# Performance work log

Measured on AMD Instinct MI355X. Metric: run time of the kernel, lower is better.

## Reference

```python
import math
import jax, jax.numpy as jnp
import numpy as np

D_MODEL = 512
NHEAD = 8
D_HEAD = D_MODEL // NHEAD
TEMP = 0.8
B, LQ, LK = 16, 512, 1024
NEG = -1.0e9


def setup_inputs() -> dict:
    key = jax.random.key(0)
    ks = jax.random.split(key, 12)
    s = 1.0 / math.sqrt(D_MODEL)
    return {
        "Q_src": jax.random.normal(ks[0], (B, LQ, D_MODEL), jnp.float32),
        "KV_src": jax.random.normal(ks[1], (B, LK, D_MODEL), jnp.float32),
        "key_gate": jax.random.uniform(ks[2], (B, LK), jnp.float32, 1e-3, 1.0),
        "key_padding_mask": jax.random.randint(ks[3], (B, LK), 0, 2, jnp.int32),
        "Wq": jax.random.normal(ks[4], (D_MODEL, D_MODEL), jnp.float32) * s,
        "bq": jnp.zeros((D_MODEL,), jnp.float32),
        "Wk": jax.random.normal(ks[5], (D_MODEL, D_MODEL), jnp.float32) * s,
        "bk": jnp.zeros((D_MODEL,), jnp.float32),
        "Wv": jax.random.normal(ks[6], (D_MODEL, D_MODEL), jnp.float32) * s,
        "bv": jnp.zeros((D_MODEL,), jnp.float32),
        "Wo": jax.random.normal(ks[7], (D_MODEL, D_MODEL), jnp.float32) * s,
        "bo": jnp.zeros((D_MODEL,), jnp.float32),
    }


def reference(Q_src, KV_src, key_gate, key_padding_mask, Wq, bq, Wk, bk, Wv, bv, Wo, bo):
    b, lq, _ = Q_src.shape
    lk = KV_src.shape[1]
    # projections -> [B, H, L, Dh]
    q = (Q_src @ Wq + bq).reshape(b, lq, NHEAD, D_HEAD).transpose(0, 2, 1, 3)
    k = (KV_src @ Wk + bk).reshape(b, lk, NHEAD, D_HEAD).transpose(0, 2, 1, 3)
    v = (KV_src @ Wv + bv).reshape(b, lk, NHEAD, D_HEAD).transpose(0, 2, 1, 3)
    # scores with log-gate bias [B, H, Lq, Lk]
    logits = jnp.einsum("bhqd,bhkd->bhqk", q, k) / math.sqrt(D_HEAD)
    logits = logits + jnp.log(key_gate)[:, None, None, :]
    pad = (key_padding_mask == 0)[:, None, None, :]
    logits = jnp.where(pad, NEG, logits) / TEMP
    attn = jax.nn.softmax(logits, axis=-1)
    ctx = jnp.einsum("bhqk,bhkd->bhqd", attn, v)
    ctx = ctx.transpose(0, 2, 1, 3).reshape(b, lq, D_MODEL)
    return ctx @ Wo + bo
```

## Files before the change

### kernel.cpp

```cpp
#include <hip/hip_runtime.h>
#include <math.h>

typedef __bf16 bf16;
typedef __bf16 bf16x8 __attribute__((ext_vector_type(8)));
typedef __bf16 bf16x4 __attribute__((ext_vector_type(4)));
typedef __bf16 bf16x2 __attribute__((ext_vector_type(2)));
typedef float  f32x4  __attribute__((ext_vector_type(4)));
typedef unsigned int uint;

#define SCQ2 0.22542110f
#define SMREF 16.0f

#define VMC(n) asm volatile("s_waitcnt vmcnt(" #n ")" ::: "memory")
#define BARR do { __builtin_amdgcn_s_barrier(); __builtin_amdgcn_sched_barrier(0); } while (0)

#if __has_builtin(__builtin_amdgcn_exp2f)
#define EXP2F __builtin_amdgcn_exp2f
#else
#define EXP2F exp2f
#endif

__device__ __forceinline__ void gload16(const void* g, void* l) {
  __builtin_amdgcn_global_load_lds((const __attribute__((address_space(1))) void*)g,
                                   (__attribute__((address_space(3))) void*)l, 16, 0, 0);
}

__device__ __forceinline__ uint pk2(float a, float b) {
  bf16x2 t = {(bf16)a, (bf16)b};
  return __builtin_bit_cast(uint, t);
}

union V8 { bf16x8 v; bf16x4 h[2]; uint u[4]; };

__global__ void prep_k(const float* __restrict__ Wq, const float* __restrict__ Wk,
                       const float* __restrict__ Wv, const float* __restrict__ Wo,
                       bf16* __restrict__ Tq, bf16* __restrict__ Tkv, bf16* __restrict__ To,
                       const float* __restrict__ gate, const int* __restrict__ mask,
                       float* __restrict__ gfac,
                       const float* __restrict__ Qs, const float* __restrict__ KVs,
                       bf16* __restrict__ Qsb, bf16* __restrict__ KVb) {
  const int bid = blockIdx.x, tid = threadIdx.x;
  if (bid < 256) {
    const int w = bid >> 6, t = bid & 63;
    const float* W = (w == 0) ? Wq : (w == 1) ? Wk : (w == 2) ? Wv : Wo;
    bf16* T = (w == 0) ? Tq : (w == 3) ? To : Tkv;
    const int ro = (w == 2) ? 512 : 0;
    const int k0 = (t >> 3) * 64, n0 = (t & 7) * 64;
    __shared__ bf16 tl[64][72];
#pragma unroll
    for (int i = 0; i < 16; i++) {
      int s = i * 256 + tid;
      int r = s >> 6, c = s & 63;
      tl[r][c] = (bf16)W[(size_t)(k0 + r) * 512 + n0 + c];
    }
    __syncthreads();
#pragma unroll
    for (int i = 0; i < 16; i++) {
      int s = i * 256 + tid;
      int r = s >> 6, c = s & 63;
      T[(size_t)(ro + n0 + r) * 512 + k0 + c] = tl[c][r];
    }
  } else if (bid < 320) {
    int i = (bid - 256) * 256 + tid;
    gfac[i] = mask[i] ? __expf(1.25f * __logf(gate[i])) : 0.0f;
  } else {
    const float* s;
    bf16* d;
    size_t i;
    if (bid < 2368) { s = Qs; d = Qsb; i = ((size_t)(bid - 320) * 256 + tid) * 8; }
    else            { s = KVs; d = KVb; i = ((size_t)(bid - 2368) * 256 + tid) * 8; }
    f32x4 a = *(const f32x4*)(s + i);
    f32x4 b = *(const f32x4*)(s + i + 4);
    bf16x8 o = {(bf16)a[0], (bf16)a[1], (bf16)a[2], (bf16)a[3],
                (bf16)b[0], (bf16)b[1], (bf16)b[2], (bf16)b[3]};
    *(bf16x8*)(d + i) = o;
  }
}

__global__ __launch_bounds__(512, 2) void gemm_kv8(
    const bf16* __restrict__ A, const bf16* __restrict__ Bt,
    const float* __restrict__ kb, const float* __restrict__ vb,
    const float* __restrict__ gfac, bf16* __restrict__ K_out, bf16* __restrict__ V_out) {
  const int tid = threadIdx.x, w = tid >> 6, l = tid & 63;
  const int lg = l >> 4, lr = l & 15;
  const int bid = (int)(blockIdx.x & 7) * 32 + (int)(blockIdx.x >> 3);
  const int bm = (bid >> 2) * 256;
  const int bn = (bid & 3) * 256;
  const int wm = w >> 2, wn = w & 3;

  __shared__ __align__(16) bf16 AB[2][16384];

  const int lrow = l >> 2;
  const int cs = (l & 3) ^ ((l >> 3) & 3);

  f32x4 acc[8][4];
#pragma unroll
  for (int i = 0; i < 8; i++)
#pragma unroll
    for (int j = 0; j < 4; j++) acc[i][j] = (f32x4){0.f, 0.f, 0.f, 0.f};

  auto stA = [&](int p, int u, int kt) {
    const int rb = (w >> 2) * 128 + u * 64 + (w & 3) * 16;
    gload16(A + (size_t)(bm + rb + lrow) * 512 + kt * 32 + cs * 8, &AB[p][rb * 32]);
  };
  auto stB = [&](int p, int u, int kt) {
    const int rb = (w >> 1) * 64 + u * 32 + (w & 1) * 16;
    gload16(Bt + (size_t)(bn + rb + lrow) * 512 + kt * 32 + cs * 8, &AB[p][8192 + rb * 32]);
  };

  bf16x8 aA[4], bb0[2], bb1[2];
#define RDA(p, mh)                                                                   \
  _Pragma("unroll") for (int m2 = 0; m2 < 4; m2++) {                                 \
    const int row = wm * 128 + (mh) * 64 + m2 * 16 + lr;                             \
    aA[m2] = *(const bf16x8*)(&AB[p][row * 32 + ((lg ^ ((row >> 1) & 3)) * 8)]);     \
  }
#define RDB(p, nh, dst)                                                              \
  _Pragma("unroll") for (int n2 = 0; n2 < 2; n2++) {                                 \
    const int row = wn * 64 + (nh) * 32 + n2 * 16 + lr;                              \
    dst[n2] = *(const bf16x8*)(&AB[p][8192 + row * 32 + ((lg ^ ((row >> 1) & 3)) * 8)]); \
  }
#define MM(mh, nh, bbv)                                                              \
  __builtin_amdgcn_s_setprio(1);                                                     \
  _Pragma("unroll") for (int m2 = 0; m2 < 4; m2++)                                   \
  _Pragma("unroll") for (int n2 = 0; n2 < 2; n2++)                                   \
    acc[(mh) * 4 + m2][(nh) * 2 + n2] =                                              \
        __builtin_amdgcn_mfma_f32_16x16x32_bf16(aA[m2], bbv[n2],                     \
                                                acc[(mh) * 4 + m2][(nh) * 2 + n2], 0, 0, 0); \
  __builtin_amdgcn_s_setprio(0);

  stA(0, 0, 0); stB(0, 0, 0); stA(0, 1, 0); stB(0, 1, 0);
  stA(1, 0, 1); stB(1, 0, 1);
  VMC(4);
  BARR;

  for (int i = 0; i < 8; ++i) {
    const bool last = (i == 7);
    const int k1 = 2 * i + 1, k2 = 2 * i + 2, k3 = 2 * i + 3;
    stA(1, 1, k1); stB(1, 1, k1);
    RDA(0, 0); RDB(0, 0, bb0);
    MM(0, 0, bb0);
    VMC(4); BARR;
    RDB(0, 1, bb1);
    MM(0, 1, bb1);
    BARR;
    if (!last) stA(0, 0, k2);
    RDA(0, 1);
    MM(1, 0, bb0);
    BARR;
    if (!last) stB(0, 0, k2);
    MM(1, 1, bb1);
    if (last) { VMC(2); } else { VMC(4); }
    BARR;
    if (!last) { stA(0, 1, k2); stB(0, 1, k2); }
    RDA(1, 0); RDB(1, 0, bb0);
    MM(0, 0, bb0);
    if (last) { VMC(0); } else { VMC(4); }
    BARR;
    RDB(1, 1, bb1);
    MM(0, 1, bb1);
    BARR;
    if (!last) stA(1, 0, k3);
    RDA(1, 1);
    MM(1, 0, bb0);
    BARR;
    if (!last) stB(1, 0, k3);
    MM(1, 1, bb1);
    VMC(4); BARR;
  }
#undef RDA
#undef RDB
#undef MM

  if (bn < 512) {
#pragma unroll
    for (int mf = 0; mf < 8; mf++) {
#pragma unroll
      for (int nf = 0; nf < 4; nf++) {
        f32x4 c = acc[mf][nf];
        const int n = bn + wn * 64 + nf * 16 + lr;
        const int m0 = bm + wm * 128 + mf * 16 + lg * 4;
        const float bias = kb[n];
#pragma unroll
        for (int r = 0; r < 4; r++) K_out[(size_t)(m0 + r) * 512 + n] = (bf16)(c[r] + bias);
      }
    }
  } else {
#pragma unroll
    for (int mf = 0; mf < 8; mf++) {
#pragma unroll
      for (int nf = 0; nf < 4; nf++) {
        f32x4 c = acc[mf][nf];
        const int n = bn + wn * 64 + nf * 16 + lr;
        const int m0 = bm + wm * 128 + mf * 16 + lg * 4;
        const int nn = n - 512;
        const int hh = nn >> 6, dd = nn & 63;
        const int bb = m0 >> 10, key = m0 & 1023;
        const int u = key & 31;
        const int keyp = (key & ~31) + ((u & 15) >> 2) * 8 + ((u >> 4) & 1) * 4;
        const float bias = vb[nn];
        f32x4 g4 = *(const f32x4*)(gfac + m0);
        bf16x4 w4 = {(bf16)((c[0] + bias) * g4[0]), (bf16)((c[1] + bias) * g4[1]),
                     (bf16)((c[2] + bias) * g4[2]), (bf16)((c[3] + bias) * g4[3])};
        *(bf16x4*)(V_out + ((size_t)((bb * 8 + hh) * 64 + dd)) * 1024 + keyp) = w4;
      }
    }
  }
}

template <int OM, int NT, int CHUNK>
__global__ __launch_bounds__(256, 2) void gemm_k(
    const bf16* __restrict__ A, const bf16* __restrict__ Bt,
    const float* __restrict__ b0, void* __restrict__ C0, float scale) {
  const int tid = threadIdx.x, w = tid >> 6, l = tid & 63;
  const int lg = l >> 4, lr = l & 15;
  const int bid = (int)(blockIdx.x & 7) * CHUNK + (int)(blockIdx.x >> 3);
  const int bm = (bid / NT) * 64;
  const int bn = (bid % NT) * 128;
  const int wr = (w >> 1) * 32, wc = (w & 1) * 64;
  __shared__ __align__(16) bf16 As[3][64][32];
  __shared__ __align__(16) bf16 Bs[3][128][32];
  const int r16 = l >> 2;
  const int cs = (l & 3) ^ ((l >> 3) & 3);

  f32x4 acc[2][4];
#pragma unroll
  for (int i = 0; i < 2; i++)
#pragma unroll
    for (int j = 0; j < 4; j++) acc[i][j] = (f32x4){0.f, 0.f, 0.f, 0.f};

  auto stage = [&](int buf, int kt) {
    gload16(A + (size_t)(bm + w * 16 + r16) * 512 + kt * 32 + cs * 8, &As[buf][w * 16][0]);
#pragma unroll
    for (int j = 0; j < 2; j++)
      gload16(Bt + (size_t)(bn + w * 32 + j * 16 + r16) * 512 + kt * 32 + cs * 8,
              &Bs[buf][w * 32 + j * 16][0]);
  };

  stage(0, 0);
  stage(1, 1);
  for (int t = 0; t < 16; ++t) {
    const int buf = t % 3;
    if (t == 15) { VMC(0); } else { VMC(3); }
    BARR;
    if (t < 14) stage((t + 2) % 3, t + 2);
    bf16x8 af[2], bfr[4];
#pragma unroll
    for (int mf = 0; mf < 2; mf++) {
      const int row = wr + mf * 16 + lr;
      af[mf] = *(const bf16x8*)(&As[buf][row][(lg ^ ((row >> 1) & 3)) * 8]);
    }
#pragma unroll
    for (int nf = 0; nf < 4; nf++) {
      const int row = wc + nf * 16 + lr;
      bfr[nf] = *(const bf16x8*)(&Bs[buf][row][(lg ^ ((row >> 1) & 3)) * 8]);
    }
    __builtin_amdgcn_s_setprio(1);
#pragma unroll
    for (int mf = 0; mf < 2; mf++)
#pragma unroll
      for (int nf = 0; nf < 4; nf++)
        acc[mf][nf] = __builtin_amdgcn_mfma_f32_16x16x32_bf16(af[mf], bfr[nf], acc[mf][nf], 0, 0, 0);
    __builtin_amdgcn_s_setprio(0);
  }

#pragma unroll
  for (int mf = 0; mf < 2; mf++) {
#pragma unroll
    for (int nf = 0; nf < 4; nf++) {
      f32x4 c = acc[mf][nf];
      const int n = bn + wc + nf * 16 + lr;
      const int m0 = bm + wr + mf * 16 + lg * 4;
      const float bias = b0[n];
      if constexpr (OM == 0) {
        bf16* C = (bf16*)C0;
#pragma unroll
        for (int r = 0; r < 4; r++) C[(size_t)(m0 + r) * 512 + n] = (bf16)((c[r] + bias) * scale);
      } else {
        float* C = (float*)C0;
#pragma unroll
        for (int r = 0; r < 4; r++) C[(size_t)(m0 + r) * 512 + n] = c[r] + bias;
      }
    }
  }
}

__global__ __launch_bounds__(256, 2) void attn_k(
    const bf16* __restrict__ Q, const bf16* __restrict__ Kb,
    const bf16* __restrict__ Vt, const float* __restrict__ gfac,
    bf16* __restrict__ ctx) {
  const int tid = threadIdx.x, w = tid >> 6, l = tid & 63;
  const int lg = l >> 4, lr = l & 15;
  const int bid = (int)(blockIdx.x & 7) * 64 + (int)(blockIdx.x >> 3);
  const int qb = bid & 3, h = (bid >> 2) & 7, b = bid >> 5;
  const int q0 = qb * 128;

  __shared__ __align__(16) bf16 Ks[3][64][64];
  __shared__ __align__(16) bf16 Vs[3][64][64];
  __shared__ __align__(16) float gfs[1024];

  bf16x8 qf[2][2];
#pragma unroll
  for (int s = 0; s < 2; s++) {
    const bf16* qp = Q + (size_t)(b * 512 + q0 + w * 32 + s * 16 + lr) * 512 + h * 64;
    qf[s][0] = *(const bf16x8*)(qp + lg * 8);
    qf[s][1] = *(const bf16x8*)(qp + 32 + lg * 8);
  }

  f32x4 o[2][4];
#pragma unroll
  for (int s = 0; s < 2; s++)
#pragma unroll
    for (int i = 0; i < 4; i++) o[s][i] = (f32x4){0.f, 0.f, 0.f, 0.f};
  f32x4 lacc[2] = {(f32x4){0.f, 0.f, 0.f, 0.f}, (f32x4){0.f, 0.f, 0.f, 0.f}};

  const int r8 = l >> 3;
  const int c8g = (l & 7) ^ ((l >> 3) & 7);
  const bf16* Kbase = Kb + ((size_t)b * 1024) * 512 + h * 64 + c8g * 8;
  const bf16* Vbase = Vt + ((size_t)(b * 8 + h) * 64) * 1024 + c8g * 8;

  auto stage = [&](int buf, int t) {
    const int kv0 = t * 64;
    gload16(Kbase + (size_t)(kv0 + w * 16 + r8) * 512, &Ks[buf][w * 16][0]);
    gload16(Kbase + (size_t)(kv0 + w * 16 + 8 + r8) * 512, &Ks[buf][w * 16 + 8][0]);
    gload16(Vbase + (size_t)(w * 16 + r8) * 1024 + kv0, &Vs[buf][w * 16][0]);
    gload16(Vbase + (size_t)(w * 16 + 8 + r8) * 1024 + kv0, &Vs[buf][w * 16 + 8][0]);
  };

  gload16(gfac + b * 1024 + w * 256 + l * 4, &gfs[w * 256]);
  stage(0, 0);
  stage(1, 1);

  for (int t = 0; t < 16; ++t) {
    const int buf = t % 3;
    if (t == 15) { VMC(0); } else { VMC(4); }
    BARR;
    if (t < 14) stage((t + 2) % 3, t + 2);

    f32x4 gvv[4];
#pragma unroll
    for (int f = 0; f < 4; f++) gvv[f] = *(const f32x4*)(&gfs[t * 64 + f * 16 + lg * 4]);

    f32x4 s4[2][4];
    __builtin_amdgcn_s_setprio(1);
#pragma unroll
    for (int f = 0; f < 4; f++) {
      const int row = f * 16 + lr;
      const bf16x8 k0 = *(const bf16x8*)(&Ks[buf][row][(lg ^ (row & 7)) * 8]);
      const bf16x8 k1 = *(const bf16x8*)(&Ks[buf][row][((4 + lg) ^ (row & 7)) * 8]);
#pragma unroll
      for (int s = 0; s < 2; s++) {
        f32x4 z = (f32x4){0.f, 0.f, 0.f, 0.f};
        z = __builtin_amdgcn_mfma_f32_16x16x32_bf16(k0, qf[s][0], z, 0, 0, 0);
        s4[s][f] = __builtin_amdgcn_mfma_f32_16x16x32_bf16(k1, qf[s][1], z, 0, 0, 0);
      }
    }
    __builtin_amdgcn_s_setprio(0);

    V8 pb[2][2];
#pragma unroll
    for (int s = 0; s < 2; s++) {
      float p[4][4];
#pragma unroll
      for (int f = 0; f < 4; f++)
#pragma unroll
        for (int r = 0; r < 4; r++) p[f][r] = EXP2F(s4[s][f][r] - SMREF);
#pragma unroll
      for (int f = 0; f < 4; f++)
#pragma unroll
        for (int r = 0; r < 4; r++) lacc[s][r] = fmaf(p[f][r], gvv[f][r], lacc[s][r]);
      pb[s][0].u[0] = pk2(p[0][0], p[0][1]); pb[s][0].u[1] = pk2(p[0][2], p[0][3]);
      pb[s][0].u[2] = pk2(p[1][0], p[1][1]); pb[s][0].u[3] = pk2(p[1][2], p[1][3]);
      pb[s][1].u[0] = pk2(p[2][0], p[2][1]); pb[s][1].u[1] = pk2(p[2][2], p[2][3]);
      pb[s][1].u[2] = pk2(p[3][0], p[3][1]); pb[s][1].u[3] = pk2(p[3][2], p[3][3]);
    }

    __builtin_amdgcn_s_setprio(1);
#pragma unroll
    for (int od = 0; od < 4; od++) {
      const int row = od * 16 + lr;
      const bf16x8 va0 = *(const bf16x8*)(&Vs[buf][row][(lg ^ (row & 7)) * 8]);
      const bf16x8 va1 = *(const bf16x8*)(&Vs[buf][row][((4 + lg) ^ (row & 7)) * 8]);
#pragma unroll
      for (int s = 0; s < 2; s++) {
        o[s][od] = __builtin_amdgcn_mfma_f32_16x16x32_bf16(va0, pb[s][0].v, o[s][od], 0, 0, 0);
        o[s][od] = __builtin_amdgcn_mfma_f32_16x16x32_bf16(va1, pb[s][1].v, o[s][od], 0, 0, 0);
      }
    }
    __builtin_amdgcn_s_setprio(0);
  }

#pragma unroll
  for (int s = 0; s < 2; s++) {
    float lp = (lacc[s][0] + lacc[s][1]) + (lacc[s][2] + lacc[s][3]);
    lp += __shfl_xor(lp, 16);
    lp += __shfl_xor(lp, 32);
    const float inv = 1.0f / lp;
    bf16* cp = ctx + (size_t)(b * 512 + q0 + w * 32 + s * 16 + lr) * 512 + h * 64;
#pragma unroll
    for (int od = 0; od < 4; od++)
#pragma unroll
      for (int r = 0; r < 4; r++) cp[od * 16 + lg * 4 + r] = (bf16)(o[s][od][r] * inv);
  }
}

extern "C" void kernel_launch(void* const* d_in, const int* in_sizes, int n_in,
                              void* d_out, int out_size, void* d_ws, size_t ws_size,
                              hipStream_t stream) {
  (void)in_sizes; (void)n_in; (void)out_size; (void)ws_size;
  const float* Q_src = (const float*)d_in[0];
  const float* KV_src = (const float*)d_in[1];
  const float* gate = (const float*)d_in[2];
  const int* mask = (const int*)d_in[3];
  const float* Wq = (const float*)d_in[4];
  const float* bq = (const float*)d_in[5];
  const float* Wk = (const float*)d_in[6];
  const float* bk = (const float*)d_in[7];
  const float* Wv = (const float*)d_in[8];
  const float* bv = (const float*)d_in[9];
  const float* Wo = (const float*)d_in[10];
  const float* bo = (const float*)d_in[11];
  float* out = (float*)d_out;

  char* ws = (char*)d_ws;
  size_t off = 0;
  auto alloc = [&](size_t bytes) {
    char* p = ws + off;
    off += (bytes + 255) & ~(size_t)255;
    return p;
  };
  bf16* Wtq = (bf16*)alloc(512 * 512 * 2);
  bf16* Btkv = (bf16*)alloc(1024 * 512 * 2);
  bf16* Wto = (bf16*)alloc(512 * 512 * 2);
  float* gfac = (float*)alloc(16384 * 4);
  bf16* Qsb = (bf16*)alloc((size_t)8192 * 512 * 2);
  bf16* KVb = (bf16*)alloc((size_t)16384 * 512 * 2);
  bf16* Qb = (bf16*)alloc((size_t)8192 * 512 * 2);
  bf16* Kb = (bf16*)alloc((size_t)16384 * 512 * 2);
  bf16* Vt = (bf16*)alloc((size_t)16384 * 512 * 2);
  bf16* Cx = KVb;

  prep_k<<<6464, 256, 0, stream>>>(Wq, Wk, Wv, Wo, Wtq, Btkv, Wto, gate, mask, gfac,
                                   Q_src, KV_src, Qsb, KVb);
  gemm_kv8<<<256, 512, 0, stream>>>(KVb, Btkv, bk, bv, gfac, Kb, Vt);
  gemm_k<0, 4, 64><<<512, 256, 0, stream>>>(Qsb, Wtq, bq, Qb, SCQ2);
  attn_k<<<512, 256, 0, stream>>>(Qb, Kb, Vt, gfac, Cx);
  gemm_k<2, 4, 64><<<512, 256, 0, stream>>>(Cx, Wto, bo, out, 1.0f);
}
```

Baseline: 86.03 us.

## Software-pipeline PV MFMA one tile behind QK to overlap exp with matmul

Restructures the attention loop so each iteration computes the QK scores for tile t, then the PV MFMAs for tile t-1 using probabilities kept from the previous iteration, then the exp/pack for tile t. A tail step after the loop handles the last PV tile. The V buffer ring grows from 3 to 4 slots so tile t-1's V is not overwritten while it is still in use. The goal is to let the exp2/pack VALU work overlap with matrix-core work instead of serialising them. The cost is more LDS and registers held live across iterations, which may hurt occupancy at 2 blocks per CU.

```diff
diff --git a/kernel.cpp b/kernel.cpp
--- a/kernel.cpp
+++ b/kernel.cpp
@@ -295,7 +295,7 @@
   const int q0 = qb * 128;
 
   __shared__ __align__(16) bf16 Ks[3][64][64];
-  __shared__ __align__(16) bf16 Vs[3][64][64];
+  __shared__ __align__(16) bf16 Vs[4][64][64];
   __shared__ __align__(16) float gfs[1024];
 
   bf16x8 qf[2][2];
@@ -312,29 +312,32 @@
 #pragma unroll
     for (int i = 0; i < 4; i++) o[s][i] = (f32x4){0.f, 0.f, 0.f, 0.f};
   f32x4 lacc[2] = {(f32x4){0.f, 0.f, 0.f, 0.f}, (f32x4){0.f, 0.f, 0.f, 0.f}};
+  V8 pb[2][2];
 
   const int r8 = l >> 3;
   const int c8g = (l & 7) ^ ((l >> 3) & 7);
   const bf16* Kbase = Kb + ((size_t)b * 1024) * 512 + h * 64 + c8g * 8;
   const bf16* Vbase = Vt + ((size_t)(b * 8 + h) * 64) * 1024 + c8g * 8;
 
-  auto stage = [&](int buf, int t) {
+  auto stage = [&](int t) {
     const int kv0 = t * 64;
-    gload16(Kbase + (size_t)(kv0 + w * 16 + r8) * 512, &Ks[buf][w * 16][0]);
-    gload16(Kbase + (size_t)(kv0 + w * 16 + 8 + r8) * 512, &Ks[buf][w * 16 + 8][0]);
-    gload16(Vbase + (size_t)(w * 16 + r8) * 1024 + kv0, &Vs[buf][w * 16][0]);
-    gload16(Vbase + (size_t)(w * 16 + 8 + r8) * 1024 + kv0, &Vs[buf][w * 16 + 8][0]);
+    bf16* kd = &Ks[t % 3][w * 16][0];
+    bf16* vd = &Vs[t & 3][w * 16][0];
+    gload16(Kbase + (size_t)(kv0 + w * 16 + r8) * 512, kd);
+    gload16(Kbase + (size_t)(kv0 + w * 16 + 8 + r8) * 512, kd + 8 * 64);
+    gload16(Vbase + (size_t)(w * 16 + r8) * 1024 + kv0, vd);
+    gload16(Vbase + (size_t)(w * 16 + 8 + r8) * 1024 + kv0, vd + 8 * 64);
   };
 
   gload16(gfac + b * 1024 + w * 256 + l * 4, &gfs[w * 256]);
-  stage(0, 0);
-  stage(1, 1);
+  stage(0);
+  stage(1);
 
   for (int t = 0; t < 16; ++t) {
-    const int buf = t % 3;
+    const int kbuf = t % 3;
     if (t == 15) { VMC(0); } else { VMC(4); }
     BARR;
-    if (t < 14) stage((t + 2) % 3, t + 2);
+    if (t < 14) stage(t + 2);
 
     f32x4 gvv[4];
 #pragma unroll
@@ -345,8 +348,8 @@
 #pragma unroll
     for (int f = 0; f < 4; f++) {
       const int row = f * 16 + lr;
-      const bf16x8 k0 = *(const bf16x8*)(&Ks[buf][row][(lg ^ (row & 7)) * 8]);
-      const bf16x8 k1 = *(const bf16x8*)(&Ks[buf][row][((4 + lg) ^ (row & 7)) * 8]);
+      const bf16x8 k0 = *(const bf16x8*)(&Ks[kbuf][row][(lg ^ (row & 7)) * 8]);
+      const bf16x8 k1 = *(const bf16x8*)(&Ks[kbuf][row][((4 + lg) ^ (row & 7)) * 8]);
 #pragma unroll
       for (int s = 0; s < 2; s++) {
         f32x4 z = (f32x4){0.f, 0.f, 0.f, 0.f};
@@ -354,9 +357,23 @@
         s4[s][f] = __builtin_amdgcn_mfma_f32_16x16x32_bf16(k1, qf[s][1], z, 0, 0, 0);
       }
     }
+
+    if (t > 0) {
+      const int vbuf = (t - 1) & 3;
+#pragma unroll
+      for (int od = 0; od < 4; od++) {
+        const int row = od * 16 + lr;
+        const bf16x8 va0 = *(const bf16x8*)(&Vs[vbuf][row][(lg ^ (row & 7)) * 8]);
+        const bf16x8 va1 = *(const bf16x8*)(&Vs[vbuf][row][((4 + lg) ^ (row & 7)) * 8]);
+#pragma unroll
+        for (int s = 0; s < 2; s++) {
+          o[s][od] = __builtin_amdgcn_mfma_f32_16x16x32_bf16(va0, pb[s][0].v, o[s][od], 0, 0, 0);
+          o[s][od] = __builtin_amdgcn_mfma_f32_16x16x32_bf16(va1, pb[s][1].v, o[s][od], 0, 0, 0);
+        }
+      }
+    }
     __builtin_amdgcn_s_setprio(0);
 
-    V8 pb[2][2];
 #pragma unroll
     for (int s = 0; s < 2; s++) {
       float p[4][4];
@@ -373,21 +390,21 @@
       pb[s][1].u[0] = pk2(p[2][0], p[2][1]); pb[s][1].u[1] = pk2(p[2][2], p[2][3]);
       pb[s][1].u[2] = pk2(p[3][0], p[3][1]); pb[s][1].u[3] = pk2(p[3][2], p[3][3]);
     }
-
-    __builtin_amdgcn_s_setprio(1);
-#pragma unroll
-    for (int od = 0; od < 4; od++) {
-      const int row = od * 16 + lr;
-      const bf16x8 va0 = *(const bf16x8*)(&Vs[buf][row][(lg ^ (row & 7)) * 8]);
-      const bf16x8 va1 = *(const bf16x8*)(&Vs[buf][row][((4 + lg) ^ (row & 7)) * 8]);
-#pragma unroll
-      for (int s = 0; s < 2; s++) {
-        o[s][od] = __builtin_amdgcn_mfma_f32_16x16x32_bf16(va0, pb[s][0].v, o[s][od], 0, 0, 0);
-        o[s][od] = __builtin_amdgcn_mfma_f32_16x16x32_bf16(va1, pb[s][1].v, o[s][od], 0, 0, 0);
-      }
-    }
-    __builtin_amdgcn_s_setprio(0);
-  }
+  }
+
+  __builtin_amdgcn_s_setprio(1);
+#pragma unroll
+  for (int od = 0; od < 4; od++) {
+    const int row = od * 16 + lr;
+    const bf16x8 va0 = *(const bf16x8*)(&Vs[3][row][(lg ^ (row & 7)) * 8]);
+    const bf16x8 va1 = *(const bf16x8*)(&Vs[3][row][((4 + lg) ^ (row & 7)) * 8]);
+#pragma unroll
+    for (int s = 0; s < 2; s++) {
+      o[s][od] = __builtin_amdgcn_mfma_f32_16x16x32_bf16(va0, pb[s][0].v, o[s][od], 0, 0, 0);
+      o[s][od] = __builtin_amdgcn_mfma_f32_16x16x32_bf16(va1, pb[s][1].v, o[s][od], 0, 0, 0);
+    }
+  }
+  __builtin_amdgcn_s_setprio(0);
 
 #pragma unroll
   for (int s = 0; s < 2; s++) {
```

After: 86.31 us. Within noise of the previous version (+0.3%).

## Split attention KV sequence across two wave groups with LDS reduction

Applied to the files above, without the earlier changes.

The attention kernel now runs 512 threads per block, and two groups of four waves each handle half of the 1024 keys for the same 128 queries. A group switches from triple to double buffering over 8 tiles of its half. The partial outputs and row sums are combined through LDS at the end. This raises the number of waves in flight and halves the serial loop length per block. In exchange it adds a reduction step and barriers, and the shallower pipeline waits on vmcnt(0) every iteration.

```diff
diff --git a/kernel.cpp b/kernel.cpp
--- a/kernel.cpp
+++ b/kernel.cpp
@@ -284,24 +284,25 @@
   }
 }
 
-__global__ __launch_bounds__(256, 2) void attn_k(
+__global__ __launch_bounds__(512, 4) void attn_k(
     const bf16* __restrict__ Q, const bf16* __restrict__ Kb,
     const bf16* __restrict__ Vt, const float* __restrict__ gfac,
     bf16* __restrict__ ctx) {
   const int tid = threadIdx.x, w = tid >> 6, l = tid & 63;
   const int lg = l >> 4, lr = l & 15;
+  const int ks = w >> 2, wl = w & 3;
   const int bid = (int)(blockIdx.x & 7) * 64 + (int)(blockIdx.x >> 3);
   const int qb = bid & 3, h = (bid >> 2) & 7, b = bid >> 5;
   const int q0 = qb * 128;
 
-  __shared__ __align__(16) bf16 Ks[3][64][64];
-  __shared__ __align__(16) bf16 Vs[3][64][64];
+  __shared__ __align__(16) bf16 Ks[2][2][64][64];
+  __shared__ __align__(16) bf16 Vs[2][2][64][64];
   __shared__ __align__(16) float gfs[1024];
 
   bf16x8 qf[2][2];
 #pragma unroll
   for (int s = 0; s < 2; s++) {
-    const bf16* qp = Q + (size_t)(b * 512 + q0 + w * 32 + s * 16 + lr) * 512 + h * 64;
+    const bf16* qp = Q + (size_t)(b * 512 + q0 + wl * 32 + s * 16 + lr) * 512 + h * 64;
     qf[s][0] = *(const bf16x8*)(qp + lg * 8);
     qf[s][1] = *(const bf16x8*)(qp + 32 + lg * 8);
   }
@@ -319,34 +320,36 @@
   const bf16* Vbase = Vt + ((size_t)(b * 8 + h) * 64) * 1024 + c8g * 8;
 
   auto stage = [&](int buf, int t) {
-    const int kv0 = t * 64;
-    gload16(Kbase + (size_t)(kv0 + w * 16 + r8) * 512, &Ks[buf][w * 16][0]);
-    gload16(Kbase + (size_t)(kv0 + w * 16 + 8 + r8) * 512, &Ks[buf][w * 16 + 8][0]);
-    gload16(Vbase + (size_t)(w * 16 + r8) * 1024 + kv0, &Vs[buf][w * 16][0]);
-    gload16(Vbase + (size_t)(w * 16 + 8 + r8) * 1024 + kv0, &Vs[buf][w * 16 + 8][0]);
+    const int kv0 = ks * 512 + t * 64;
+    bf16* kd = &Ks[ks][buf][wl * 16][0];
+    bf16* vd = &Vs[ks][buf][wl * 16][0];
+    gload16(Kbase + (size_t)(kv0 + wl * 16 + r8) * 512, kd);
+    gload16(Kbase + (size_t)(kv0 + wl * 16 + 8 + r8) * 512, kd + 8 * 64);
+    gload16(Vbase + (size_t)(wl * 16 + r8) * 1024 + kv0, vd);
+    gload16(Vbase + (size_t)(wl * 16 + 8 + r8) * 1024 + kv0, vd + 8 * 64);
   };
 
-  gload16(gfac + b * 1024 + w * 256 + l * 4, &gfs[w * 256]);
+  if (w < 4) gload16(gfac + b * 1024 + w * 256 + l * 4, &gfs[w * 256]);
   stage(0, 0);
-  stage(1, 1);
-
-  for (int t = 0; t < 16; ++t) {
-    const int buf = t % 3;
-    if (t == 15) { VMC(0); } else { VMC(4); }
-    BARR;
-    if (t < 14) stage((t + 2) % 3, t + 2);
+
+  for (int t = 0; t < 8; ++t) {
+    const int buf = t & 1;
+    VMC(0);
+    BARR;
+    if (t < 7) stage(buf ^ 1, t + 1);
 
     f32x4 gvv[4];
 #pragma unroll
-    for (int f = 0; f < 4; f++) gvv[f] = *(const f32x4*)(&gfs[t * 64 + f * 16 + lg * 4]);
+    for (int f = 0; f < 4; f++)
+      gvv[f] = *(const f32x4*)(&gfs[ks * 512 + t * 64 + f * 16 + lg * 4]);
 
     f32x4 s4[2][4];
     __builtin_amdgcn_s_setprio(1);
 #pragma unroll
     for (int f = 0; f < 4; f++) {
       const int row = f * 16 + lr;
-      const bf16x8 k0 = *(const bf16x8*)(&Ks[buf][row][(lg ^ (row & 7)) * 8]);
-      const bf16x8 k1 = *(const bf16x8*)(&Ks[buf][row][((4 + lg) ^ (row & 7)) * 8]);
+      const bf16x8 k0 = *(const bf16x8*)(&Ks[ks][buf][row][(lg ^ (row & 7)) * 8]);
+      const bf16x8 k1 = *(const bf16x8*)(&Ks[ks][buf][row][((4 + lg) ^ (row & 7)) * 8]);
 #pragma unroll
       for (int s = 0; s < 2; s++) {
         f32x4 z = (f32x4){0.f, 0.f, 0.f, 0.f};
@@ -378,8 +381,8 @@
 #pragma unroll
     for (int od = 0; od < 4; od++) {
       const int row = od * 16 + lr;
-      const bf16x8 va0 = *(const bf16x8*)(&Vs[buf][row][(lg ^ (row & 7)) * 8]);
-      const bf16x8 va1 = *(const bf16x8*)(&Vs[buf][row][((4 + lg) ^ (row & 7)) * 8]);
+      const bf16x8 va0 = *(const bf16x8*)(&Vs[ks][buf][row][(lg ^ (row & 7)) * 8]);
+      const bf16x8 va1 = *(const bf16x8*)(&Vs[ks][buf][row][((4 + lg) ^ (row & 7)) * 8]);
 #pragma unroll
       for (int s = 0; s < 2; s++) {
         o[s][od] = __builtin_amdgcn_mfma_f32_16x16x32_bf16(va0, pb[s][0].v, o[s][od], 0, 0, 0);
@@ -389,17 +392,39 @@
     __builtin_amdgcn_s_setprio(0);
   }
 
-#pragma unroll
-  for (int s = 0; s < 2; s++) {
-    float lp = (lacc[s][0] + lacc[s][1]) + (lacc[s][2] + lacc[s][3]);
-    lp += __shfl_xor(lp, 16);
-    lp += __shfl_xor(lp, 32);
-    const float inv = 1.0f / lp;
-    bf16* cp = ctx + (size_t)(b * 512 + q0 + w * 32 + s * 16 + lr) * 512 + h * 64;
-#pragma unroll
-    for (int od = 0; od < 4; od++)
-#pragma unroll
-      for (int r = 0; r < 4; r++) cp[od * 16 + lg * 4 + r] = (bf16)(o[s][od][r] * inv);
+  f32x4* Om = (f32x4*)&Ks[0][0][0][0];
+  f32x4* Lm = (f32x4*)&Vs[0][0][0][0];
+  __syncthreads();
+  if (ks == 1) {
+#pragma unroll
+    for (int s = 0; s < 2; s++)
+#pragma unroll
+      for (int od = 0; od < 4; od++)
+        Om[(wl * 64 + l) * 8 + ((s * 4 + od) ^ (l & 7))] = o[s][od];
+    Lm[(wl * 64 + l) * 2] = lacc[0];
+    Lm[(wl * 64 + l) * 2 + 1] = lacc[1];
+  }
+  __syncthreads();
+  if (ks == 0) {
+#pragma unroll
+    for (int s = 0; s < 2; s++)
+#pragma unroll
+      for (int od = 0; od < 4; od++)
+        o[s][od] += Om[(wl * 64 + l) * 8 + ((s * 4 + od) ^ (l & 7))];
+    lacc[0] += Lm[(wl * 64 + l) * 2];
+    lacc[1] += Lm[(wl * 64 + l) * 2 + 1];
+#pragma unroll
+    for (int s = 0; s < 2; s++) {
+      float lp = (lacc[s][0] + lacc[s][1]) + (lacc[s][2] + lacc[s][3]);
+      lp += __shfl_xor(lp, 16);
+      lp += __shfl_xor(lp, 32);
+      const float inv = 1.0f / lp;
+      bf16* cp = ctx + (size_t)(b * 512 + q0 + wl * 32 + s * 16 + lr) * 512 + h * 64;
+#pragma unroll
+      for (int od = 0; od < 4; od++)
+#pragma unroll
+        for (int r = 0; r < 4; r++) cp[od * 16 + lg * 4 + r] = (bf16)(o[s][od][r] * inv);
+    }
   }
 }
 
@@ -443,6 +468,6 @@
                                    Q_src, KV_src, Qsb, KVb);
   gemm_kv8<<<256, 512, 0, stream>>>(KVb, Btkv, bk, bv, gfac, Kb, Vt);
   gemm_k<0, 4, 64><<<512, 256, 0, stream>>>(Qsb, Wtq, bq, Qb, SCQ2);
-  attn_k<<<512, 256, 0, stream>>>(Qb, Kb, Vt, gfac, Cx);
+  attn_k<<<512, 512, 0, stream>>>(Qb, Kb, Vt, gfac, Cx);
   gemm_k<2, 4, 64><<<512, 256, 0, stream>>>(Cx, Wto, bo, out, 1.0f);
 }
```

Result: slower. 88.26 us (+2.6%).

## Switch attention KV pipeline to double-buffered 128-key tiles and fold max offset into MFMA

Applied to the files above, without the earlier changes.

Replaces the 3-stage 64-key ring buffer with two 128-key buffers, each split into two 64-key sub-tiles. The next tile is prefetched while both sub-tiles are computed, so there is one wait and barrier per 128 keys instead of one per 64. The fixed softmax offset is now applied by initialising the score accumulator to -SMREF rather than subtracting it before exp2. In exchange, shared memory per block grows from 3 to 4 64x64 tiles each for K and V. The full wait at the end of each iteration also removes the slack the deeper prefetch gave.

```diff
diff --git a/kernel.cpp b/kernel.cpp
--- a/kernel.cpp
+++ b/kernel.cpp
@@ -294,8 +294,8 @@
   const int qb = bid & 3, h = (bid >> 2) & 7, b = bid >> 5;
   const int q0 = qb * 128;
 
-  __shared__ __align__(16) bf16 Ks[3][64][64];
-  __shared__ __align__(16) bf16 Vs[3][64][64];
+  __shared__ __align__(16) bf16 Ks[2][2][64][64];
+  __shared__ __align__(16) bf16 Vs[2][2][64][64];
   __shared__ __align__(16) float gfs[1024];
 
   bf16x8 qf[2][2];
@@ -319,74 +319,85 @@
   const bf16* Vbase = Vt + ((size_t)(b * 8 + h) * 64) * 1024 + c8g * 8;
 
   auto stage = [&](int buf, int t) {
-    const int kv0 = t * 64;
-    gload16(Kbase + (size_t)(kv0 + w * 16 + r8) * 512, &Ks[buf][w * 16][0]);
-    gload16(Kbase + (size_t)(kv0 + w * 16 + 8 + r8) * 512, &Ks[buf][w * 16 + 8][0]);
-    gload16(Vbase + (size_t)(w * 16 + r8) * 1024 + kv0, &Vs[buf][w * 16][0]);
-    gload16(Vbase + (size_t)(w * 16 + 8 + r8) * 1024 + kv0, &Vs[buf][w * 16 + 8][0]);
+#pragma unroll
+    for (int sub = 0; sub < 2; sub++) {
+      const int kv0 = t * 128 + sub * 64;
+      bf16* kd = &Ks[buf][sub][w * 16][0];
+      bf16* vd = &Vs[buf][sub][w * 16][0];
+      gload16(Kbase + (size_t)(kv0 + w * 16 + r8) * 512, kd);
+      gload16(Kbase + (size_t)(kv0 + w * 16 + 8 + r8) * 512, kd + 8 * 64);
+      gload16(Vbase + (size_t)(w * 16 + r8) * 1024 + kv0, vd);
+      gload16(Vbase + (size_t)(w * 16 + 8 + r8) * 1024 + kv0, vd + 8 * 64);
+    }
   };
 
   gload16(gfac + b * 1024 + w * 256 + l * 4, &gfs[w * 256]);
   stage(0, 0);
-  stage(1, 1);
-
-  for (int t = 0; t < 16; ++t) {
-    const int buf = t % 3;
-    if (t == 15) { VMC(0); } else { VMC(4); }
-    BARR;
-    if (t < 14) stage((t + 2) % 3, t + 2);
-
-    f32x4 gvv[4];
-#pragma unroll
-    for (int f = 0; f < 4; f++) gvv[f] = *(const f32x4*)(&gfs[t * 64 + f * 16 + lg * 4]);
-
-    f32x4 s4[2][4];
-    __builtin_amdgcn_s_setprio(1);
-#pragma unroll
-    for (int f = 0; f < 4; f++) {
-      const int row = f * 16 + lr;
-      const bf16x8 k0 = *(const bf16x8*)(&Ks[buf][row][(lg ^ (row & 7)) * 8]);
-      const bf16x8 k1 = *(const bf16x8*)(&Ks[buf][row][((4 + lg) ^ (row & 7)) * 8]);
+  VMC(0);
+  BARR;
+
+  for (int t = 0; t < 8; ++t) {
+    const int buf = t & 1;
+    if (t < 7) stage(buf ^ 1, t + 1);
+
+#pragma unroll
+    for (int sub = 0; sub < 2; sub++) {
+      f32x4 gvv[4];
+#pragma unroll
+      for (int f = 0; f < 4; f++)
+        gvv[f] = *(const f32x4*)(&gfs[t * 128 + sub * 64 + f * 16 + lg * 4]);
+
+      f32x4 s4[2][4];
+      __builtin_amdgcn_s_setprio(1);
+#pragma unroll
+      for (int f = 0; f < 4; f++) {
+        const int row = f * 16 + lr;
+        const bf16x8 k0 = *(const bf16x8*)(&Ks[buf][sub][row][(lg ^ (row & 7)) * 8]);
+        const bf16x8 k1 = *(const bf16x8*)(&Ks[buf][sub][row][((4 + lg) ^ (row & 7)) * 8]);
+#pragma unroll
+        for (int s = 0; s < 2; s++) {
+          f32x4 z = (f32x4){-SMREF, -SMREF, -SMREF, -SMREF};
+          z = __builtin_amdgcn_mfma_f32_16x16x32_bf16(k0, qf[s][0], z, 0, 0, 0);
+          s4[s][f] = __builtin_amdgcn_mfma_f32_16x16x32_bf16(k1, qf[s][1], z, 0, 0, 0);
+        }
+      }
+      __builtin_amdgcn_s_setprio(0);
+
+      V8 pb[2][2];
 #pragma unroll
       for (int s = 0; s < 2; s++) {
-        f32x4 z = (f32x4){0.f, 0.f, 0.f, 0.f};
-        z = __builtin_amdgcn_mfma_f32_16x16x32_bf16(k0, qf[s][0], z, 0, 0, 0);
-        s4[s][f] = __builtin_amdgcn_mfma_f32_16x16x32_bf16(k1, qf[s][1], z, 0, 0, 0);
-      }
-    }
-    __builtin_amdgcn_s_setprio(0);
-
-    V8 pb[2][2];
-#pragma unroll
-    for (int s = 0; s < 2; s++) {
-      float p[4][4];
-#pragma unroll
-      for (int f = 0; f < 4; f++)
-#pragma unroll
-        for (int r = 0; r < 4; r++) p[f][r] = EXP2F(s4[s][f][r] - SMREF);
-#pragma unroll
-      for (int f = 0; f < 4; f++)
-#pragma unroll
-        for (int r = 0; r < 4; r++) lacc[s][r] = fmaf(p[f][r], gvv[f][r], lacc[s][r]);
-      pb[s][0].u[0] = pk2(p[0][0], p[0][1]); pb[s][0].u[1] = pk2(p[0][2], p[0][3]);
-      pb[s][0].u[2] = pk2(p[1][0], p[1][1]); pb[s][0].u[3] = pk2(p[1][2], p[1][3]);
-      pb[s][1].u[0] = pk2(p[2][0], p[2][1]); pb[s][1].u[1] = pk2(p[2][2], p[2][3]);
-      pb[s][1].u[2] = pk2(p[3][0], p[3][1]); pb[s][1].u[3] = pk2(p[3][2], p[3][3]);
-    }
-
-    __builtin_amdgcn_s_setprio(1);
-#pragma unroll
-    for (int od = 0; od < 4; od++) {
-      const int row = od * 16 + lr;
-      const bf16x8 va0 = *(const bf16x8*)(&Vs[buf][row][(lg ^ (row & 7)) * 8]);
-      const bf16x8 va1 = *(const bf16x8*)(&Vs[buf][row][((4 + lg) ^ (row & 7)) * 8]);
-#pragma unroll
-      for (int s = 0; s < 2; s++) {
-        o[s][od] = __builtin_amdgcn_mfma_f32_16x16x32_bf16(va0, pb[s][0].v, o[s][od], 0, 0, 0);
-        o[s][od] = __builtin_amdgcn_mfma_f32_16x16x32_bf16(va1, pb[s][1].v, o[s][od], 0, 0, 0);
-      }
-    }
-    __builtin_amdgcn_s_setprio(0);
+        float p[4][4];
+#pragma unroll
+        for (int f = 0; f < 4; f++)
+#pragma unroll
+          for (int r = 0; r < 4; r++) p[f][r] = EXP2F(s4[s][f][r]);
+#pragma unroll
+        for (int f = 0; f < 4; f++)
+#pragma unroll
+          for (int r = 0; r < 4; r++) lacc[s][r] = fmaf(p[f][r], gvv[f][r], lacc[s][r]);
+        pb[s][0].u[0] = pk2(p[0][0], p[0][1]); pb[s][0].u[1] = pk2(p[0][2], p[0][3]);
+        pb[s][0].u[2] = pk2(p[1][0], p[1][1]); pb[s][0].u[3] = pk2(p[1][2], p[1][3]);
+        pb[s][1].u[0] = pk2(p[2][0], p[2][1]); pb[s][1].u[1] = pk2(p[2][2], p[2][3]);
+        pb[s][1].u[2] = pk2(p[3][0], p[3][1]); pb[s][1].u[3] = pk2(p[3][2], p[3][3]);
+      }
+
+      __builtin_amdgcn_s_setprio(1);
+#pragma unroll
+      for (int od = 0; od < 4; od++) {
+        const int row = od * 16 + lr;
+        const bf16x8 va0 = *(const bf16x8*)(&Vs[buf][sub][row][(lg ^ (row & 7)) * 8]);
+        const bf16x8 va1 = *(const bf16x8*)(&Vs[buf][sub][row][((4 + lg) ^ (row & 7)) * 8]);
+#pragma unroll
+        for (int s = 0; s < 2; s++) {
+          o[s][od] = __builtin_amdgcn_mfma_f32_16x16x32_bf16(va0, pb[s][0].v, o[s][od], 0, 0, 0);
+          o[s][od] = __builtin_amdgcn_mfma_f32_16x16x32_bf16(va1, pb[s][1].v, o[s][od], 0, 0, 0);
+        }
+      }
+      __builtin_amdgcn_s_setprio(0);
+    }
+
+    if (t < 7) VMC(0);
+    BARR;
   }
 
 #pragma unroll
```

Result: no change. 85.60 us (-0.5%).
